# Kernel tuning notes

Hardware: AMD Instinct MI355X
Metric: run time of the kernel (lower is better)

Reference implementation:

```python
import jax, jax.numpy as jnp
import numpy as np

N_NODES = 100000
N_EDGES = 3200000
D = 16
L = 3


def setup_inputs() -> dict:
    key = jax.random.key(0)
    ks = jax.random.split(key, 7)
    scale = 1.0 / np.sqrt(D)
    x = jax.random.normal(ks[0], (N_NODES, D), dtype=jnp.float32)
    edge_index = jax.random.randint(ks[1], (2, N_EDGES), 0, N_NODES, dtype=jnp.int64)
    Wl = jax.random.normal(ks[2], (L, D, D), dtype=jnp.float32) * scale
    bl = jax.random.normal(ks[3], (L, D), dtype=jnp.float32) * scale
    Wr = jax.random.normal(ks[4], (L, D, D), dtype=jnp.float32) * scale
    Wlin = jax.random.normal(ks[5], (L, D, D), dtype=jnp.float32) * scale
    blin = jax.random.normal(ks[6], (L, D), dtype=jnp.float32) * scale
    return {"x": x, "edge_index": edge_index, "Wl": Wl, "bl": bl,
            "Wr": Wr, "Wlin": Wlin, "blin": blin}


def reference(x, edge_index, Wl, bl, Wr, Wlin, blin):
    src = edge_index[0]
    dst = edge_index[1]
    n = x.shape[0]
    # in-degree for mean aggregation (PyG SAGEConv aggr='mean')
    deg = jax.ops.segment_sum(jnp.ones((src.shape[0],), dtype=x.dtype), dst,
                              num_segments=n)
    denom = jnp.maximum(deg, 1.0)[:, None]  # nodes with no in-edges -> 0 agg
    for i in range(Wl.shape[0]):
        # gather source features, scatter-mean onto targets
        agg = jax.ops.segment_sum(x[src], dst, num_segments=n) / denom
        conv = agg @ Wl[i].T + bl[i] + x @ Wr[i].T  # SAGEConv: lin_l(agg)+lin_r(x)
        x = conv + x @ Wlin[i].T + blin[i]          # + Linear residual
    return x
```

## Files before the change

### kernel.cpp

```cpp
#include <hip/hip_runtime.h>

#define N_NODES 100000
#define N_EDGES 3200000
#define D 16
#define L 3

#define TILE 128
#define NB ((N_NODES + TILE - 1) / TILE)
#define CAP 4608
#define NBLK 500
#define SEG (N_EDGES / NBLK)
#define BINT 1024
#define LT 512

__device__ __forceinline__ unsigned packbf(float a, float b) {
    unsigned ua = __float_as_uint(a); ua += 0x7FFFu + ((ua >> 16) & 1u);
    unsigned ub = __float_as_uint(b); ub += 0x7FFFu + ((ub >> 16) & 1u);
    return (ua >> 16) | (ub & 0xFFFF0000u);
}
#define BLO(u) __uint_as_float((u) << 16)
#define BHI(u) __uint_as_float((u) & 0xFFFF0000u)

__global__ void cvt_kernel(const float* __restrict__ x, unsigned* __restrict__ xbf,
                           int* __restrict__ cursor, int n4) {
    int t = blockIdx.x * blockDim.x + threadIdx.x;
    if (t < NB) cursor[t] = 0;
    if (t >= n4) return;
    float4 v = *(const float4*)(x + (size_t)t * 4);
    uint2 o; o.x = packbf(v.x, v.y); o.y = packbf(v.z, v.w);
    *(uint2*)(xbf + (size_t)t * 2) = o;
}

__global__ void bin_scatter(const int* __restrict__ src, const int* __restrict__ dst,
                            int* __restrict__ cursor, unsigned* __restrict__ ebuf, int E) {
    __shared__ int lcnt[NB];
    __shared__ int ldiff[NB];
    __shared__ int lofs[NB];
    __shared__ unsigned sorted[SEG];
    __shared__ unsigned short sbkt[SEG];
    int tid = threadIdx.x;
    for (int i = tid; i < NB; i += BINT) lcnt[i] = 0;
    __syncthreads();
    int b0 = blockIdx.x * SEG, b1 = min(E, b0 + SEG);
    for (int e = b0 + tid * 4; e < b1; e += BINT * 4) {
        int4 d4 = *(const int4*)(dst + e);
        atomicAdd(&lcnt[d4.x >> 7], 1);
        atomicAdd(&lcnt[d4.y >> 7], 1);
        atomicAdd(&lcnt[d4.z >> 7], 1);
        atomicAdd(&lcnt[d4.w >> 7], 1);
    }
    __syncthreads();
    {
        int v = (tid < NB) ? lcnt[tid] : 0;
        sorted[tid] = (unsigned)v;
        __syncthreads();
        for (int off = 1; off < BINT; off <<= 1) {
            unsigned t = (tid >= off) ? sorted[tid - off] : 0u;
            __syncthreads();
            sorted[tid] += t;
            __syncthreads();
        }
        if (tid < NB) {
            int incl = (int)sorted[tid];
            int excl = incl - v;
            lofs[tid] = excl;
            int g = v ? (tid * CAP + atomicAdd(&cursor[tid], v)) : 0;
            ldiff[tid] = g - excl;
            lcnt[tid] = excl;
        }
        __syncthreads();
    }
    for (int e = b0 + tid * 4; e < b1; e += BINT * 4) {
        int4 d4 = *(const int4*)(dst + e);
        int4 s4 = *(const int4*)(src + e);
        int b_, pos;
        b_ = d4.x >> 7; pos = atomicAdd(&lcnt[b_], 1);
        sorted[pos] = ((unsigned)(d4.x & 127) << 17) | (unsigned)s4.x; sbkt[pos] = (unsigned short)b_;
        b_ = d4.y >> 7; pos = atomicAdd(&lcnt[b_], 1);
        sorted[pos] = ((unsigned)(d4.y & 127) << 17) | (unsigned)s4.y; sbkt[pos] = (unsigned short)b_;
        b_ = d4.z >> 7; pos = atomicAdd(&lcnt[b_], 1);
        sorted[pos] = ((unsigned)(d4.z & 127) << 17) | (unsigned)s4.z; sbkt[pos] = (unsigned short)b_;
        b_ = d4.w >> 7; pos = atomicAdd(&lcnt[b_], 1);
        sorted[pos] = ((unsigned)(d4.w & 127) << 17) | (unsigned)s4.w; sbkt[pos] = (unsigned short)b_;
    }
    __syncthreads();
    int nLoc = b1 - b0;
    for (int i = tid; i < nLoc; i += BINT) {
        int b_ = sbkt[i];
        ebuf[ldiff[b_] + i] = sorted[i];
    }
}

__device__ __forceinline__ void agg_xform(
    const float* __restrict__ xin, const unsigned* __restrict__ xbf,
    const unsigned* se2, const int* lofs, int n_loc,
    const float* sWl, const float* sWc, const float* sbc,
    float* __restrict__ xout, unsigned* __restrict__ xbf_out,
    int emit_bf, int b, int N, int tid) {
    int q = tid & 3;
    int n = b * TILE + n_loc;
    if (n >= N) return;

    int s0 = lofs[n_loc];
    int s1 = lofs[n_loc + 1];
    int deg = s1 - s0;

    int lane2 = q >> 1;
    int ho = (q & 1) * 4;

    float acc[8] = {0.f,0.f,0.f,0.f,0.f,0.f,0.f,0.f};
    float bcc[8] = {0.f,0.f,0.f,0.f,0.f,0.f,0.f,0.f};
    int i = s0;
    for (; i + 8 <= s1; i += 8) {
        unsigned p0 = se2[i + 0 + lane2] & 0x1FFFF;
        unsigned p1 = se2[i + 2 + lane2] & 0x1FFFF;
        unsigned p2 = se2[i + 4 + lane2] & 0x1FFFF;
        unsigned p3 = se2[i + 6 + lane2] & 0x1FFFF;
        uint4 g0 = *(const uint4*)(xbf + (size_t)p0 * 8 + ho);
        uint4 g1 = *(const uint4*)(xbf + (size_t)p1 * 8 + ho);
        uint4 g2 = *(const uint4*)(xbf + (size_t)p2 * 8 + ho);
        uint4 g3 = *(const uint4*)(xbf + (size_t)p3 * 8 + ho);
        acc[0] += BLO(g0.x); acc[1] += BHI(g0.x); acc[2] += BLO(g0.y); acc[3] += BHI(g0.y);
        acc[4] += BLO(g0.z); acc[5] += BHI(g0.z); acc[6] += BLO(g0.w); acc[7] += BHI(g0.w);
        bcc[0] += BLO(g1.x); bcc[1] += BHI(g1.x); bcc[2] += BLO(g1.y); bcc[3] += BHI(g1.y);
        bcc[4] += BLO(g1.z); bcc[5] += BHI(g1.z); bcc[6] += BLO(g1.w); bcc[7] += BHI(g1.w);
        acc[0] += BLO(g2.x); acc[1] += BHI(g2.x); acc[2] += BLO(g2.y); acc[3] += BHI(g2.y);
        acc[4] += BLO(g2.z); acc[5] += BHI(g2.z); acc[6] += BLO(g2.w); acc[7] += BHI(g2.w);
        bcc[0] += BLO(g3.x); bcc[1] += BHI(g3.x); bcc[2] += BLO(g3.y); bcc[3] += BHI(g3.y);
        bcc[4] += BLO(g3.z); bcc[5] += BHI(g3.z); bcc[6] += BLO(g3.w); bcc[7] += BHI(g3.w);
    }
    for (; i + 2 <= s1; i += 2) {
        unsigned p = se2[i + lane2] & 0x1FFFF;
        uint4 g = *(const uint4*)(xbf + (size_t)p * 8 + ho);
        acc[0] += BLO(g.x); acc[1] += BHI(g.x); acc[2] += BLO(g.y); acc[3] += BHI(g.y);
        acc[4] += BLO(g.z); acc[5] += BHI(g.z); acc[6] += BLO(g.w); acc[7] += BHI(g.w);
    }
    if (i < s1 && lane2 == 0) {
        unsigned p = se2[i] & 0x1FFFF;
        uint4 g = *(const uint4*)(xbf + (size_t)p * 8 + ho);
        acc[0] += BLO(g.x); acc[1] += BHI(g.x); acc[2] += BLO(g.y); acc[3] += BHI(g.y);
        acc[4] += BLO(g.z); acc[5] += BHI(g.z); acc[6] += BLO(g.w); acc[7] += BHI(g.w);
    }
    #pragma unroll
    for (int k = 0; k < 8; k++) acc[k] += bcc[k];
    #pragma unroll
    for (int k = 0; k < 8; k++) acc[k] += __shfl_xor(acc[k], 2, 4);

    int srcAbs = (tid & 63 & ~3) | (q >> 1);
    float inv = 1.0f / fmaxf((float)deg, 1.0f);
    float a[4];
    #pragma unroll
    for (int k = 0; k < 4; k++) {
        float lo = __shfl(acc[k], srcAbs);
        float hi = __shfl(acc[4 + k], srcAbs);
        a[k] = ((q & 1) ? hi : lo) * inv;
    }

    float4 xq = *(const float4*)(xin + (size_t)n * D + q * 4);
    float xv[4] = { xq.x, xq.y, xq.z, xq.w };

    float o[4];
    #pragma unroll
    for (int j = 0; j < D; j++) {
        float p = 0.f;
        #pragma unroll
        for (int k = 0; k < 4; k++) {
            int kk = q * 4 + k;
            p += a[k] * sWl[j * D + kk] + xv[k] * sWc[j * D + kk];
        }
        p += __shfl_xor(p, 1, 4);
        p += __shfl_xor(p, 2, 4);
        if ((j >> 2) == q) o[j & 3] = p + sbc[j];
    }
    *(float4*)(xout + (size_t)n * D + q * 4) = make_float4(o[0], o[1], o[2], o[3]);
    if (emit_bf) {
        uint2 ob; ob.x = packbf(o[0], o[1]); ob.y = packbf(o[2], o[3]);
        *(uint2*)(xbf_out + (size_t)n * 8 + q * 2) = ob;
    }
}

__global__ void layer0_kernel(const float* __restrict__ xin, const unsigned* __restrict__ xbf,
                              unsigned* __restrict__ ebuf, const int* __restrict__ cnt,
                              int* __restrict__ node_start, int* __restrict__ gperm,
                              const float* __restrict__ Wl, const float* __restrict__ bl,
                              const float* __restrict__ Wr, const float* __restrict__ Wlin,
                              const float* __restrict__ blin,
                              float* __restrict__ xout, unsigned* __restrict__ xbf_out, int N) {
    __shared__ unsigned se[CAP];
    __shared__ unsigned se2[CAP];
    __shared__ int lcnt[TILE];
    __shared__ int sscan[TILE];
    __shared__ int lofs[TILE + 1];
    __shared__ int sdeg[TILE];
    __shared__ int perm[TILE];
    __shared__ float sWl[D * D];
    __shared__ float sWc[D * D];
    __shared__ float sbc[D];

    int tid = threadIdx.x;
    int b = blockIdx.x;
    int base = b * CAP;
    int nE = min(cnt[b], CAP);

    if (tid < D * D) { sWl[tid] = Wl[tid]; sWc[tid] = Wr[tid] + Wlin[tid]; }
    if (tid < D) sbc[tid] = bl[tid] + blin[tid];
    if (tid < TILE) lcnt[tid] = 0;
    __syncthreads();
    for (int i = tid; i < nE; i += LT) {
        unsigned p = ebuf[base + i];
        se[i] = p;
        atomicAdd(&lcnt[p >> 17], 1);
    }
    __syncthreads();
    if (tid < TILE) sscan[tid] = lcnt[tid];
    __syncthreads();
    for (int off = 1; off < TILE; off <<= 1) {
        int t = (tid < TILE && tid >= off) ? sscan[tid - off] : 0;
        __syncthreads();
        if (tid < TILE) sscan[tid] += t;
        __syncthreads();
    }
    if (tid < TILE) {
        int excl = sscan[tid] - lcnt[tid];
        lofs[tid] = excl;
        lcnt[tid] = excl;
        sdeg[tid] = sscan[tid] - excl;
        node_start[b * TILE + tid] = excl;
        if (tid == TILE - 1) lofs[TILE] = sscan[tid];
    }
    __syncthreads();
    if (tid < TILE) {
        int dm = sdeg[tid];
        int r = 0;
        for (int j = 0; j < TILE; j++) {
            int dj = sdeg[j];
            r += (dj > dm) || (dj == dm && j < tid);
        }
        perm[r] = tid;
        gperm[b * TILE + r] = tid;
    }
    for (int i = tid; i < nE; i += LT) {
        unsigned p = se[i];
        int pos = atomicAdd(&lcnt[p >> 17], 1);
        se2[pos] = p;
    }
    __syncthreads();
    for (int i = tid; i < nE; i += LT)
        ebuf[base + i] = se2[i];

    agg_xform(xin, xbf, se2, lofs, perm[tid >> 2], sWl, sWc, sbc,
              xout, xbf_out, 1, b, N, tid);
}

__global__ void layerN_kernel(const float* __restrict__ xin, const unsigned* __restrict__ xbf,
                              const unsigned* __restrict__ ebuf, const int* __restrict__ cnt,
                              const int* __restrict__ node_start, const int* __restrict__ gperm,
                              const float* __restrict__ Wl, const float* __restrict__ bl,
                              const float* __restrict__ Wr, const float* __restrict__ Wlin,
                              const float* __restrict__ blin,
                              float* __restrict__ xout, unsigned* __restrict__ xbf_out,
                              int emit_bf, int N) {
    __shared__ unsigned se2[CAP];
    __shared__ int lofs[TILE + 1];
    __shared__ float sWl[D * D];
    __shared__ float sWc[D * D];
    __shared__ float sbc[D];

    int tid = threadIdx.x;
    int b = blockIdx.x;
    int base = b * CAP;
    int nE = min(cnt[b], CAP);

    if (tid < D * D) { sWl[tid] = Wl[tid]; sWc[tid] = Wr[tid] + Wlin[tid]; }
    if (tid < D) sbc[tid] = bl[tid] + blin[tid];
    if (tid < TILE) lofs[tid] = node_start[b * TILE + tid];
    if (tid == 0) lofs[TILE] = nE;
    for (int i = tid; i < nE; i += LT) se2[i] = ebuf[base + i];
    int n_loc = gperm[b * TILE + (tid >> 2)];
    __syncthreads();

    agg_xform(xin, xbf, se2, lofs, n_loc, sWl, sWc, sbc,
              xout, xbf_out, emit_bf, b, N, tid);
}

extern "C" void kernel_launch(void* const* d_in, const int* in_sizes, int n_in,
                              void* d_out, int out_size, void* d_ws, size_t ws_size,
                              hipStream_t stream) {
    const float* x    = (const float*)d_in[0];
    const int*   ei   = (const int*)d_in[1];
    const float* Wl   = (const float*)d_in[2];
    const float* bl   = (const float*)d_in[3];
    const float* Wr   = (const float*)d_in[4];
    const float* Wlin = (const float*)d_in[5];
    const float* blin = (const float*)d_in[6];
    float* out = (float*)d_out;

    const int* src = ei;
    const int* dst = ei + N_EDGES;

    char* w = (char*)d_ws;
    unsigned* ebuf   = (unsigned*)w;  w += (size_t)NB * CAP * 4;
    float* bufA      = (float*)w;     w += (size_t)N_NODES * D * 4;
    float* bufB      = (float*)w;     w += (size_t)N_NODES * D * 4;
    unsigned* xbf0   = (unsigned*)w;  w += (size_t)N_NODES * 8 * 4;
    unsigned* xbf1   = (unsigned*)w;  w += (size_t)N_NODES * 8 * 4;
    int*   cursor    = (int*)w;       w += (size_t)NB * 4;
    int*   node_start= (int*)w;       w += (size_t)NB * TILE * 4;
    int*   gperm     = (int*)w;       w += (size_t)NB * TILE * 4;

    cvt_kernel<<<(N_NODES * D / 4 + 255) / 256, 256, 0, stream>>>(
        x, xbf0, cursor, N_NODES * D / 4);
    bin_scatter<<<NBLK, BINT, 0, stream>>>(src, dst, cursor, ebuf, N_EDGES);

    layer0_kernel<<<NB, LT, 0, stream>>>(
        x, xbf0, ebuf, cursor, node_start, gperm,
        Wl, bl, Wr, Wlin, blin, bufA, xbf1, N_NODES);
    layerN_kernel<<<NB, LT, 0, stream>>>(
        bufA, xbf1, ebuf, cursor, node_start, gperm,
        Wl + D * D, bl + D, Wr + D * D, Wlin + D * D, blin + D, bufB, xbf0, 1, N_NODES);
    layerN_kernel<<<NB, LT, 0, stream>>>(
        bufB, xbf0, ebuf, cursor, node_start, gperm,
        Wl + 2 * D * D, bl + 2 * D, Wr + 2 * D * D, Wlin + 2 * D * D, blin + 2 * D,
        out, xbf1, 0, N_NODES);
}
```

Measured before the change: 199.5 us.

## Shrink node tiles, fuse bf16 conversion into binning, drop fp32 intermediates

Changes the node tile from 128 to 100 with a smaller per-bucket edge capacity, so buckets use division instead of shifts and 100 of the 128 thread groups do work. Merges the bf16 conversion kernel into the binning kernel as extra blocks and zeroes the cursors with a memset. Intermediate layers now store only bf16 activations and layers 1-2 read their self features from bf16, which removes the fp32 intermediate buffer traffic but adds rounding error. Idle thread groups leave the kernel early.

```diff
diff --git a/kernel.cpp b/kernel.cpp
--- a/kernel.cpp
+++ b/kernel.cpp
@@ -5,12 +5,13 @@
 #define D 16
 #define L 3
 
-#define TILE 128
+#define TILE 100
 #define NB ((N_NODES + TILE - 1) / TILE)
-#define CAP 4608
+#define CAP 3584
 #define NBLK 500
 #define SEG (N_EDGES / NBLK)
 #define BINT 1024
+#define CVTB 391
 #define LT 512
 
 __device__ __forceinline__ unsigned packbf(float a, float b) {
@@ -21,33 +22,35 @@
 #define BLO(u) __uint_as_float((u) << 16)
 #define BHI(u) __uint_as_float((u) & 0xFFFF0000u)
 
-__global__ void cvt_kernel(const float* __restrict__ x, unsigned* __restrict__ xbf,
-                           int* __restrict__ cursor, int n4) {
-    int t = blockIdx.x * blockDim.x + threadIdx.x;
-    if (t < NB) cursor[t] = 0;
-    if (t >= n4) return;
-    float4 v = *(const float4*)(x + (size_t)t * 4);
-    uint2 o; o.x = packbf(v.x, v.y); o.y = packbf(v.z, v.w);
-    *(uint2*)(xbf + (size_t)t * 2) = o;
-}
-
-__global__ void bin_scatter(const int* __restrict__ src, const int* __restrict__ dst,
-                            int* __restrict__ cursor, unsigned* __restrict__ ebuf, int E) {
+__global__ __launch_bounds__(BINT) void pre_kernel(
+        const float* __restrict__ x, unsigned* __restrict__ xbf,
+        const int* __restrict__ src, const int* __restrict__ dst,
+        int* __restrict__ cursor, unsigned* __restrict__ ebuf, int E, int n4) {
     __shared__ int lcnt[NB];
     __shared__ int ldiff[NB];
-    __shared__ int lofs[NB];
     __shared__ unsigned sorted[SEG];
     __shared__ unsigned short sbkt[SEG];
     int tid = threadIdx.x;
+
+    if (blockIdx.x >= NBLK) {
+        int t = (blockIdx.x - NBLK) * BINT + tid;
+        if (t < n4) {
+            float4 v = *(const float4*)(x + (size_t)t * 4);
+            uint2 o; o.x = packbf(v.x, v.y); o.y = packbf(v.z, v.w);
+            *(uint2*)(xbf + (size_t)t * 2) = o;
+        }
+        return;
+    }
+
     for (int i = tid; i < NB; i += BINT) lcnt[i] = 0;
     __syncthreads();
     int b0 = blockIdx.x * SEG, b1 = min(E, b0 + SEG);
     for (int e = b0 + tid * 4; e < b1; e += BINT * 4) {
         int4 d4 = *(const int4*)(dst + e);
-        atomicAdd(&lcnt[d4.x >> 7], 1);
-        atomicAdd(&lcnt[d4.y >> 7], 1);
-        atomicAdd(&lcnt[d4.z >> 7], 1);
-        atomicAdd(&lcnt[d4.w >> 7], 1);
+        atomicAdd(&lcnt[(unsigned)d4.x / TILE], 1);
+        atomicAdd(&lcnt[(unsigned)d4.y / TILE], 1);
+        atomicAdd(&lcnt[(unsigned)d4.z / TILE], 1);
+        atomicAdd(&lcnt[(unsigned)d4.w / TILE], 1);
     }
     __syncthreads();
     {
@@ -61,9 +64,7 @@
             __syncthreads();
         }
         if (tid < NB) {
-            int incl = (int)sorted[tid];
-            int excl = incl - v;
-            lofs[tid] = excl;
+            int excl = (int)sorted[tid] - v;
             int g = v ? (tid * CAP + atomicAdd(&cursor[tid], v)) : 0;
             ldiff[tid] = g - excl;
             lcnt[tid] = excl;
@@ -73,15 +74,15 @@
     for (int e = b0 + tid * 4; e < b1; e += BINT * 4) {
         int4 d4 = *(const int4*)(dst + e);
         int4 s4 = *(const int4*)(src + e);
-        int b_, pos;
-        b_ = d4.x >> 7; pos = atomicAdd(&lcnt[b_], 1);
-        sorted[pos] = ((unsigned)(d4.x & 127) << 17) | (unsigned)s4.x; sbkt[pos] = (unsigned short)b_;
-        b_ = d4.y >> 7; pos = atomicAdd(&lcnt[b_], 1);
-        sorted[pos] = ((unsigned)(d4.y & 127) << 17) | (unsigned)s4.y; sbkt[pos] = (unsigned short)b_;
-        b_ = d4.z >> 7; pos = atomicAdd(&lcnt[b_], 1);
-        sorted[pos] = ((unsigned)(d4.z & 127) << 17) | (unsigned)s4.z; sbkt[pos] = (unsigned short)b_;
-        b_ = d4.w >> 7; pos = atomicAdd(&lcnt[b_], 1);
-        sorted[pos] = ((unsigned)(d4.w & 127) << 17) | (unsigned)s4.w; sbkt[pos] = (unsigned short)b_;
+        unsigned b_; int pos;
+        b_ = (unsigned)d4.x / TILE; pos = atomicAdd(&lcnt[b_], 1);
+        sorted[pos] = ((unsigned)(d4.x - b_ * TILE) << 17) | (unsigned)s4.x; sbkt[pos] = (unsigned short)b_;
+        b_ = (unsigned)d4.y / TILE; pos = atomicAdd(&lcnt[b_], 1);
+        sorted[pos] = ((unsigned)(d4.y - b_ * TILE) << 17) | (unsigned)s4.y; sbkt[pos] = (unsigned short)b_;
+        b_ = (unsigned)d4.z / TILE; pos = atomicAdd(&lcnt[b_], 1);
+        sorted[pos] = ((unsigned)(d4.z - b_ * TILE) << 17) | (unsigned)s4.z; sbkt[pos] = (unsigned short)b_;
+        b_ = (unsigned)d4.w / TILE; pos = atomicAdd(&lcnt[b_], 1);
+        sorted[pos] = ((unsigned)(d4.w - b_ * TILE) << 17) | (unsigned)s4.w; sbkt[pos] = (unsigned short)b_;
     }
     __syncthreads();
     int nLoc = b1 - b0;
@@ -92,7 +93,7 @@
 }
 
 __device__ __forceinline__ void agg_xform(
-    const float* __restrict__ xin, const unsigned* __restrict__ xbf,
+    const float* __restrict__ self_f32, const unsigned* __restrict__ xbf,
     const unsigned* se2, const int* lofs, int n_loc,
     const float* sWl, const float* sWc, const float* sbc,
     float* __restrict__ xout, unsigned* __restrict__ xbf_out,
@@ -156,8 +157,14 @@
         a[k] = ((q & 1) ? hi : lo) * inv;
     }
 
-    float4 xq = *(const float4*)(xin + (size_t)n * D + q * 4);
-    float xv[4] = { xq.x, xq.y, xq.z, xq.w };
+    float xv[4];
+    if (self_f32) {
+        float4 xq = *(const float4*)(self_f32 + (size_t)n * D + q * 4);
+        xv[0] = xq.x; xv[1] = xq.y; xv[2] = xq.z; xv[3] = xq.w;
+    } else {
+        uint2 gx = *(const uint2*)(xbf + (size_t)n * 8 + q * 2);
+        xv[0] = BLO(gx.x); xv[1] = BHI(gx.x); xv[2] = BLO(gx.y); xv[3] = BHI(gx.y);
+    }
 
     float o[4];
     #pragma unroll
@@ -172,20 +179,22 @@
         p += __shfl_xor(p, 2, 4);
         if ((j >> 2) == q) o[j & 3] = p + sbc[j];
     }
-    *(float4*)(xout + (size_t)n * D + q * 4) = make_float4(o[0], o[1], o[2], o[3]);
     if (emit_bf) {
         uint2 ob; ob.x = packbf(o[0], o[1]); ob.y = packbf(o[2], o[3]);
         *(uint2*)(xbf_out + (size_t)n * 8 + q * 2) = ob;
-    }
-}
-
-__global__ void layer0_kernel(const float* __restrict__ xin, const unsigned* __restrict__ xbf,
-                              unsigned* __restrict__ ebuf, const int* __restrict__ cnt,
-                              int* __restrict__ node_start, int* __restrict__ gperm,
-                              const float* __restrict__ Wl, const float* __restrict__ bl,
-                              const float* __restrict__ Wr, const float* __restrict__ Wlin,
-                              const float* __restrict__ blin,
-                              float* __restrict__ xout, unsigned* __restrict__ xbf_out, int N) {
+    } else {
+        *(float4*)(xout + (size_t)n * D + q * 4) = make_float4(o[0], o[1], o[2], o[3]);
+    }
+}
+
+__global__ __launch_bounds__(LT) void layer0_kernel(
+        const float* __restrict__ xin, const unsigned* __restrict__ xbf,
+        unsigned* __restrict__ ebuf, const int* __restrict__ cnt,
+        int* __restrict__ node_start, int* __restrict__ gperm,
+        const float* __restrict__ Wl, const float* __restrict__ bl,
+        const float* __restrict__ Wr, const float* __restrict__ Wlin,
+        const float* __restrict__ blin,
+        unsigned* __restrict__ xbf_out, int N) {
     __shared__ unsigned se[CAP];
     __shared__ unsigned se2[CAP];
     __shared__ int lcnt[TILE];
@@ -248,18 +257,22 @@
     for (int i = tid; i < nE; i += LT)
         ebuf[base + i] = se2[i];
 
-    agg_xform(xin, xbf, se2, lofs, perm[tid >> 2], sWl, sWc, sbc,
-              xout, xbf_out, 1, b, N, tid);
-}
-
-__global__ void layerN_kernel(const float* __restrict__ xin, const unsigned* __restrict__ xbf,
-                              const unsigned* __restrict__ ebuf, const int* __restrict__ cnt,
-                              const int* __restrict__ node_start, const int* __restrict__ gperm,
-                              const float* __restrict__ Wl, const float* __restrict__ bl,
-                              const float* __restrict__ Wr, const float* __restrict__ Wlin,
-                              const float* __restrict__ blin,
-                              float* __restrict__ xout, unsigned* __restrict__ xbf_out,
-                              int emit_bf, int N) {
+    int grp = tid >> 2;
+    int n_loc = (grp < TILE) ? perm[grp] : 0;
+    if (grp >= TILE) return;
+    agg_xform(xin, xbf, se2, lofs, n_loc, sWl, sWc, sbc,
+              nullptr, xbf_out, 1, b, N, tid);
+}
+
+__global__ __launch_bounds__(LT) void layerN_kernel(
+        const unsigned* __restrict__ xbf,
+        const unsigned* __restrict__ ebuf, const int* __restrict__ cnt,
+        const int* __restrict__ node_start, const int* __restrict__ gperm,
+        const float* __restrict__ Wl, const float* __restrict__ bl,
+        const float* __restrict__ Wr, const float* __restrict__ Wlin,
+        const float* __restrict__ blin,
+        float* __restrict__ xout, unsigned* __restrict__ xbf_out,
+        int emit_bf, int N) {
     __shared__ unsigned se2[CAP];
     __shared__ int lofs[TILE + 1];
     __shared__ float sWl[D * D];
@@ -276,10 +289,12 @@
     if (tid < TILE) lofs[tid] = node_start[b * TILE + tid];
     if (tid == 0) lofs[TILE] = nE;
     for (int i = tid; i < nE; i += LT) se2[i] = ebuf[base + i];
-    int n_loc = gperm[b * TILE + (tid >> 2)];
-    __syncthreads();
-
-    agg_xform(xin, xbf, se2, lofs, n_loc, sWl, sWc, sbc,
+    int grp = tid >> 2;
+    int n_loc = (grp < TILE) ? gperm[b * TILE + grp] : 0;
+    __syncthreads();
+
+    if (grp >= TILE) return;
+    agg_xform(nullptr, xbf, se2, lofs, n_loc, sWl, sWc, sbc,
               xout, xbf_out, emit_bf, b, N, tid);
 }
 
@@ -300,26 +315,25 @@
 
     char* w = (char*)d_ws;
     unsigned* ebuf   = (unsigned*)w;  w += (size_t)NB * CAP * 4;
-    float* bufA      = (float*)w;     w += (size_t)N_NODES * D * 4;
-    float* bufB      = (float*)w;     w += (size_t)N_NODES * D * 4;
     unsigned* xbf0   = (unsigned*)w;  w += (size_t)N_NODES * 8 * 4;
     unsigned* xbf1   = (unsigned*)w;  w += (size_t)N_NODES * 8 * 4;
     int*   cursor    = (int*)w;       w += (size_t)NB * 4;
     int*   node_start= (int*)w;       w += (size_t)NB * TILE * 4;
     int*   gperm     = (int*)w;       w += (size_t)NB * TILE * 4;
 
-    cvt_kernel<<<(N_NODES * D / 4 + 255) / 256, 256, 0, stream>>>(
-        x, xbf0, cursor, N_NODES * D / 4);
-    bin_scatter<<<NBLK, BINT, 0, stream>>>(src, dst, cursor, ebuf, N_EDGES);
+    hipMemsetAsync(cursor, 0, (size_t)NB * 4, stream);
+    pre_kernel<<<NBLK + CVTB, BINT, 0, stream>>>(
+        x, xbf0, src, dst, cursor, ebuf, N_EDGES, N_NODES * D / 4);
 
     layer0_kernel<<<NB, LT, 0, stream>>>(
         x, xbf0, ebuf, cursor, node_start, gperm,
-        Wl, bl, Wr, Wlin, blin, bufA, xbf1, N_NODES);
+        Wl, bl, Wr, Wlin, blin, xbf1, N_NODES);
     layerN_kernel<<<NB, LT, 0, stream>>>(
-        bufA, xbf1, ebuf, cursor, node_start, gperm,
-        Wl + D * D, bl + D, Wr + D * D, Wlin + D * D, blin + D, bufB, xbf0, 1, N_NODES);
+        xbf1, ebuf, cursor, node_start, gperm,
+        Wl + D * D, bl + D, Wr + D * D, Wlin + D * D, blin + D,
+        nullptr, xbf0, 1, N_NODES);
     layerN_kernel<<<NB, LT, 0, stream>>>(
-        bufB, xbf0, ebuf, cursor, node_start, gperm,
+        xbf0, ebuf, cursor, node_start, gperm,
         Wl + 2 * D * D, bl + 2 * D, Wr + 2 * D * D, Wlin + 2 * D * D, blin + 2 * D,
-        out, xbf1, 0, N_NODES);
-}
+        out, nullptr, 0, N_NODES);
+}
```

After: 202.6 us. No clear change (+1.6%).

## Merge convert into binning kernel, use wave-shuffle scans, software-pipeline gathers

Applied to the files above, without the earlier changes.

Folds the bf16 conversion into the binning launch as extra blocks, and replaces the cursor reset with a memset. The block-wide Hillis-Steele scans in binning and layer0 become wavefront shuffle scans. The gather loop is software-pipelined, issuing the next group of loads before accumulating the current one, and the x load is hoisted ahead of it. Edge-buffer copies are vectorized to uint4 and launch bounds are added. The intent is to cut launch count, barrier overhead and gather latency, at the cost of higher register pressure from the in-flight loads.

```diff
diff --git a/kernel.cpp b/kernel.cpp
--- a/kernel.cpp
+++ b/kernel.cpp
@@ -3,7 +3,6 @@
 #define N_NODES 100000
 #define N_EDGES 3200000
 #define D 16
-#define L 3
 
 #define TILE 128
 #define NB ((N_NODES + TILE - 1) / TILE)
@@ -11,7 +10,9 @@
 #define NBLK 500
 #define SEG (N_EDGES / NBLK)
 #define BINT 1024
+#define CVTB 391
 #define LT 512
+#define N4 (N_NODES * D / 4)
 
 __device__ __forceinline__ unsigned packbf(float a, float b) {
     unsigned ua = __float_as_uint(a); ua += 0x7FFFu + ((ua >> 16) & 1u);
@@ -21,28 +22,31 @@
 #define BLO(u) __uint_as_float((u) << 16)
 #define BHI(u) __uint_as_float((u) & 0xFFFF0000u)
 
-__global__ void cvt_kernel(const float* __restrict__ x, unsigned* __restrict__ xbf,
-                           int* __restrict__ cursor, int n4) {
-    int t = blockIdx.x * blockDim.x + threadIdx.x;
-    if (t < NB) cursor[t] = 0;
-    if (t >= n4) return;
-    float4 v = *(const float4*)(x + (size_t)t * 4);
-    uint2 o; o.x = packbf(v.x, v.y); o.y = packbf(v.z, v.w);
-    *(uint2*)(xbf + (size_t)t * 2) = o;
-}
-
-__global__ void bin_scatter(const int* __restrict__ src, const int* __restrict__ dst,
-                            int* __restrict__ cursor, unsigned* __restrict__ ebuf, int E) {
+__global__ __launch_bounds__(BINT, 8) void pre_kernel(
+        const float* __restrict__ x, unsigned* __restrict__ xbf,
+        const int* __restrict__ src, const int* __restrict__ dst,
+        int* __restrict__ cursor, unsigned* __restrict__ ebuf) {
     __shared__ int lcnt[NB];
     __shared__ int ldiff[NB];
-    __shared__ int lofs[NB];
     __shared__ unsigned sorted[SEG];
     __shared__ unsigned short sbkt[SEG];
+    __shared__ int wsum[16];
     int tid = threadIdx.x;
+
+    if (blockIdx.x >= NBLK) {
+        int t = (blockIdx.x - NBLK) * BINT + tid;
+        if (t < N4) {
+            float4 v = *(const float4*)(x + (size_t)t * 4);
+            uint2 o; o.x = packbf(v.x, v.y); o.y = packbf(v.z, v.w);
+            *(uint2*)(xbf + (size_t)t * 2) = o;
+        }
+        return;
+    }
+
     for (int i = tid; i < NB; i += BINT) lcnt[i] = 0;
     __syncthreads();
-    int b0 = blockIdx.x * SEG, b1 = min(E, b0 + SEG);
-    for (int e = b0 + tid * 4; e < b1; e += BINT * 4) {
+    int b0 = blockIdx.x * SEG;
+    for (int e = b0 + tid * 4; e < b0 + SEG; e += BINT * 4) {
         int4 d4 = *(const int4*)(dst + e);
         atomicAdd(&lcnt[d4.x >> 7], 1);
         atomicAdd(&lcnt[d4.y >> 7], 1);
@@ -51,26 +55,31 @@
     }
     __syncthreads();
     {
+        int lane = tid & 63, wv = tid >> 6;
         int v = (tid < NB) ? lcnt[tid] : 0;
-        sorted[tid] = (unsigned)v;
+        int s = v;
+        #pragma unroll
+        for (int d_ = 1; d_ < 64; d_ <<= 1) {
+            int u = __shfl_up(s, d_, 64);
+            if (lane >= d_) s += u;
+        }
+        if (lane == 63) wsum[wv] = s;
         __syncthreads();
-        for (int off = 1; off < BINT; off <<= 1) {
-            unsigned t = (tid >= off) ? sorted[tid - off] : 0u;
-            __syncthreads();
-            sorted[tid] += t;
-            __syncthreads();
-        }
+        if (tid == 0) {
+            int a = 0;
+            #pragma unroll
+            for (int i = 0; i < 16; i++) { int t_ = wsum[i]; wsum[i] = a; a += t_; }
+        }
+        __syncthreads();
+        int excl = wsum[wv] + s - v;
         if (tid < NB) {
-            int incl = (int)sorted[tid];
-            int excl = incl - v;
-            lofs[tid] = excl;
             int g = v ? (tid * CAP + atomicAdd(&cursor[tid], v)) : 0;
             ldiff[tid] = g - excl;
             lcnt[tid] = excl;
         }
         __syncthreads();
     }
-    for (int e = b0 + tid * 4; e < b1; e += BINT * 4) {
+    for (int e = b0 + tid * 4; e < b0 + SEG; e += BINT * 4) {
         int4 d4 = *(const int4*)(dst + e);
         int4 s4 = *(const int4*)(src + e);
         int b_, pos;
@@ -84,12 +93,16 @@
         sorted[pos] = ((unsigned)(d4.w & 127) << 17) | (unsigned)s4.w; sbkt[pos] = (unsigned short)b_;
     }
     __syncthreads();
-    int nLoc = b1 - b0;
-    for (int i = tid; i < nLoc; i += BINT) {
+    for (int i = tid; i < SEG; i += BINT) {
         int b_ = sbkt[i];
         ebuf[ldiff[b_] + i] = sorted[i];
     }
 }
+
+#define LDG(j) (*(const uint4*)(xbf + (size_t)(se2[(j) + lane2] & 0x1FFFF) * 8 + ho))
+#define ACC8(g) do { \
+    acc[0] += BLO((g).x); acc[1] += BHI((g).x); acc[2] += BLO((g).y); acc[3] += BHI((g).y); \
+    acc[4] += BLO((g).z); acc[5] += BHI((g).z); acc[6] += BLO((g).w); acc[7] += BHI((g).w); } while (0)
 
 __device__ __forceinline__ void agg_xform(
     const float* __restrict__ xin, const unsigned* __restrict__ xbf,
@@ -101,48 +114,36 @@
     int n = b * TILE + n_loc;
     if (n >= N) return;
 
+    float4 xq = *(const float4*)(xin + (size_t)n * D + q * 4);
+    float xv[4] = { xq.x, xq.y, xq.z, xq.w };
+
     int s0 = lofs[n_loc];
     int s1 = lofs[n_loc + 1];
     int deg = s1 - s0;
-
     int lane2 = q >> 1;
     int ho = (q & 1) * 4;
 
     float acc[8] = {0.f,0.f,0.f,0.f,0.f,0.f,0.f,0.f};
-    float bcc[8] = {0.f,0.f,0.f,0.f,0.f,0.f,0.f,0.f};
+    int end8 = s0 + (deg & ~7);
     int i = s0;
-    for (; i + 8 <= s1; i += 8) {
-        unsigned p0 = se2[i + 0 + lane2] & 0x1FFFF;
-        unsigned p1 = se2[i + 2 + lane2] & 0x1FFFF;
-        unsigned p2 = se2[i + 4 + lane2] & 0x1FFFF;
-        unsigned p3 = se2[i + 6 + lane2] & 0x1FFFF;
-        uint4 g0 = *(const uint4*)(xbf + (size_t)p0 * 8 + ho);
-        uint4 g1 = *(const uint4*)(xbf + (size_t)p1 * 8 + ho);
-        uint4 g2 = *(const uint4*)(xbf + (size_t)p2 * 8 + ho);
-        uint4 g3 = *(const uint4*)(xbf + (size_t)p3 * 8 + ho);
-        acc[0] += BLO(g0.x); acc[1] += BHI(g0.x); acc[2] += BLO(g0.y); acc[3] += BHI(g0.y);
-        acc[4] += BLO(g0.z); acc[5] += BHI(g0.z); acc[6] += BLO(g0.w); acc[7] += BHI(g0.w);
-        bcc[0] += BLO(g1.x); bcc[1] += BHI(g1.x); bcc[2] += BLO(g1.y); bcc[3] += BHI(g1.y);
-        bcc[4] += BLO(g1.z); bcc[5] += BHI(g1.z); bcc[6] += BLO(g1.w); bcc[7] += BHI(g1.w);
-        acc[0] += BLO(g2.x); acc[1] += BHI(g2.x); acc[2] += BLO(g2.y); acc[3] += BHI(g2.y);
-        acc[4] += BLO(g2.z); acc[5] += BHI(g2.z); acc[6] += BLO(g2.w); acc[7] += BHI(g2.w);
-        bcc[0] += BLO(g3.x); bcc[1] += BHI(g3.x); bcc[2] += BLO(g3.y); bcc[3] += BHI(g3.y);
-        bcc[4] += BLO(g3.z); bcc[5] += BHI(g3.z); bcc[6] += BLO(g3.w); bcc[7] += BHI(g3.w);
+    if (i < end8) {
+        uint4 c0 = LDG(i + 0), c1 = LDG(i + 2), c2 = LDG(i + 4), c3 = LDG(i + 6);
+        i += 8;
+        for (; i < end8; i += 8) {
+            uint4 n0 = LDG(i + 0), n1 = LDG(i + 2), n2 = LDG(i + 4), n3 = LDG(i + 6);
+            ACC8(c0); ACC8(c1); ACC8(c2); ACC8(c3);
+            c0 = n0; c1 = n1; c2 = n2; c3 = n3;
+        }
+        ACC8(c0); ACC8(c1); ACC8(c2); ACC8(c3);
     }
     for (; i + 2 <= s1; i += 2) {
-        unsigned p = se2[i + lane2] & 0x1FFFF;
-        uint4 g = *(const uint4*)(xbf + (size_t)p * 8 + ho);
-        acc[0] += BLO(g.x); acc[1] += BHI(g.x); acc[2] += BLO(g.y); acc[3] += BHI(g.y);
-        acc[4] += BLO(g.z); acc[5] += BHI(g.z); acc[6] += BLO(g.w); acc[7] += BHI(g.w);
+        uint4 g = LDG(i);
+        ACC8(g);
     }
     if (i < s1 && lane2 == 0) {
-        unsigned p = se2[i] & 0x1FFFF;
-        uint4 g = *(const uint4*)(xbf + (size_t)p * 8 + ho);
-        acc[0] += BLO(g.x); acc[1] += BHI(g.x); acc[2] += BLO(g.y); acc[3] += BHI(g.y);
-        acc[4] += BLO(g.z); acc[5] += BHI(g.z); acc[6] += BLO(g.w); acc[7] += BHI(g.w);
-    }
-    #pragma unroll
-    for (int k = 0; k < 8; k++) acc[k] += bcc[k];
+        uint4 g = *(const uint4*)(xbf + (size_t)(se2[i] & 0x1FFFF) * 8 + ho);
+        ACC8(g);
+    }
     #pragma unroll
     for (int k = 0; k < 8; k++) acc[k] += __shfl_xor(acc[k], 2, 4);
 
@@ -156,9 +157,6 @@
         a[k] = ((q & 1) ? hi : lo) * inv;
     }
 
-    float4 xq = *(const float4*)(xin + (size_t)n * D + q * 4);
-    float xv[4] = { xq.x, xq.y, xq.z, xq.w };
-
     float o[4];
     #pragma unroll
     for (int j = 0; j < D; j++) {
@@ -179,17 +177,17 @@
     }
 }
 
-__global__ void layer0_kernel(const float* __restrict__ xin, const unsigned* __restrict__ xbf,
-                              unsigned* __restrict__ ebuf, const int* __restrict__ cnt,
-                              int* __restrict__ node_start, int* __restrict__ gperm,
-                              const float* __restrict__ Wl, const float* __restrict__ bl,
-                              const float* __restrict__ Wr, const float* __restrict__ Wlin,
-                              const float* __restrict__ blin,
-                              float* __restrict__ xout, unsigned* __restrict__ xbf_out, int N) {
+__global__ void layer0_kernel(
+        const float* __restrict__ xin, const unsigned* __restrict__ xbf,
+        unsigned* __restrict__ ebuf, const int* __restrict__ cnt,
+        int* __restrict__ node_start, int* __restrict__ gperm,
+        const float* __restrict__ Wl, const float* __restrict__ bl,
+        const float* __restrict__ Wr, const float* __restrict__ Wlin,
+        const float* __restrict__ blin,
+        float* __restrict__ xout, unsigned* __restrict__ xbf_out, int N) {
     __shared__ unsigned se[CAP];
     __shared__ unsigned se2[CAP];
     __shared__ int lcnt[TILE];
-    __shared__ int sscan[TILE];
     __shared__ int lofs[TILE + 1];
     __shared__ int sdeg[TILE];
     __shared__ int perm[TILE];
@@ -201,32 +199,33 @@
     int b = blockIdx.x;
     int base = b * CAP;
     int nE = min(cnt[b], CAP);
+    int nE4 = (nE + 3) >> 2;
 
     if (tid < D * D) { sWl[tid] = Wl[tid]; sWc[tid] = Wr[tid] + Wlin[tid]; }
     if (tid < D) sbc[tid] = bl[tid] + blin[tid];
     if (tid < TILE) lcnt[tid] = 0;
-    __syncthreads();
-    for (int i = tid; i < nE; i += LT) {
-        unsigned p = ebuf[base + i];
-        se[i] = p;
-        atomicAdd(&lcnt[p >> 17], 1);
-    }
-    __syncthreads();
-    if (tid < TILE) sscan[tid] = lcnt[tid];
-    __syncthreads();
-    for (int off = 1; off < TILE; off <<= 1) {
-        int t = (tid < TILE && tid >= off) ? sscan[tid - off] : 0;
-        __syncthreads();
-        if (tid < TILE) sscan[tid] += t;
-        __syncthreads();
-    }
-    if (tid < TILE) {
-        int excl = sscan[tid] - lcnt[tid];
-        lofs[tid] = excl;
-        lcnt[tid] = excl;
-        sdeg[tid] = sscan[tid] - excl;
-        node_start[b * TILE + tid] = excl;
-        if (tid == TILE - 1) lofs[TILE] = sscan[tid];
+    for (int i = tid; i < nE4; i += LT)
+        ((uint4*)se)[i] = ((const uint4*)(ebuf + base))[i];
+    __syncthreads();
+    for (int i = tid; i < nE; i += LT)
+        atomicAdd(&lcnt[se[i] >> 17], 1);
+    __syncthreads();
+    if (tid < 64) {
+        int l2 = tid * 2;
+        int c0 = lcnt[l2], c1 = lcnt[l2 + 1];
+        int v = c0 + c1, s = v;
+        #pragma unroll
+        for (int d_ = 1; d_ < 64; d_ <<= 1) {
+            int u = __shfl_up(s, d_, 64);
+            if (tid >= d_) s += u;
+        }
+        int excl = s - v;
+        lofs[l2] = excl; sdeg[l2] = c0; lcnt[l2] = excl;
+        node_start[b * TILE + l2] = excl;
+        int e1 = excl + c0;
+        lofs[l2 + 1] = e1; sdeg[l2 + 1] = c1; lcnt[l2 + 1] = e1;
+        node_start[b * TILE + l2 + 1] = e1;
+        if (tid == 63) lofs[TILE] = s;
     }
     __syncthreads();
     if (tid < TILE) {
@@ -245,21 +244,22 @@
         se2[pos] = p;
     }
     __syncthreads();
-    for (int i = tid; i < nE; i += LT)
-        ebuf[base + i] = se2[i];
+    for (int i = tid; i < nE4; i += LT)
+        ((uint4*)(ebuf + base))[i] = ((const uint4*)se2)[i];
 
     agg_xform(xin, xbf, se2, lofs, perm[tid >> 2], sWl, sWc, sbc,
               xout, xbf_out, 1, b, N, tid);
 }
 
-__global__ void layerN_kernel(const float* __restrict__ xin, const unsigned* __restrict__ xbf,
-                              const unsigned* __restrict__ ebuf, const int* __restrict__ cnt,
-                              const int* __restrict__ node_start, const int* __restrict__ gperm,
-                              const float* __restrict__ Wl, const float* __restrict__ bl,
-                              const float* __restrict__ Wr, const float* __restrict__ Wlin,
-                              const float* __restrict__ blin,
-                              float* __restrict__ xout, unsigned* __restrict__ xbf_out,
-                              int emit_bf, int N) {
+__global__ __launch_bounds__(LT, 8) void layerN_kernel(
+        const float* __restrict__ xin, const unsigned* __restrict__ xbf,
+        const unsigned* __restrict__ ebuf, const int* __restrict__ cnt,
+        const int* __restrict__ node_start, const int* __restrict__ gperm,
+        const float* __restrict__ Wl, const float* __restrict__ bl,
+        const float* __restrict__ Wr, const float* __restrict__ Wlin,
+        const float* __restrict__ blin,
+        float* __restrict__ xout, unsigned* __restrict__ xbf_out,
+        int emit_bf, int N) {
     __shared__ unsigned se2[CAP];
     __shared__ int lofs[TILE + 1];
     __shared__ float sWl[D * D];
@@ -270,12 +270,14 @@
     int b = blockIdx.x;
     int base = b * CAP;
     int nE = min(cnt[b], CAP);
+    int nE4 = (nE + 3) >> 2;
 
     if (tid < D * D) { sWl[tid] = Wl[tid]; sWc[tid] = Wr[tid] + Wlin[tid]; }
     if (tid < D) sbc[tid] = bl[tid] + blin[tid];
     if (tid < TILE) lofs[tid] = node_start[b * TILE + tid];
     if (tid == 0) lofs[TILE] = nE;
-    for (int i = tid; i < nE; i += LT) se2[i] = ebuf[base + i];
+    for (int i = tid; i < nE4; i += LT)
+        ((uint4*)se2)[i] = ((const uint4*)(ebuf + base))[i];
     int n_loc = gperm[b * TILE + (tid >> 2)];
     __syncthreads();
 
@@ -308,9 +310,8 @@
     int*   node_start= (int*)w;       w += (size_t)NB * TILE * 4;
     int*   gperm     = (int*)w;       w += (size_t)NB * TILE * 4;
 
-    cvt_kernel<<<(N_NODES * D / 4 + 255) / 256, 256, 0, stream>>>(
-        x, xbf0, cursor, N_NODES * D / 4);
-    bin_scatter<<<NBLK, BINT, 0, stream>>>(src, dst, cursor, ebuf, N_EDGES);
+    hipMemsetAsync(cursor, 0, (size_t)NB * 4, stream);
+    pre_kernel<<<NBLK + CVTB, BINT, 0, stream>>>(x, xbf0, src, dst, cursor, ebuf);
 
     layer0_kernel<<<NB, LT, 0, stream>>>(
         x, xbf0, ebuf, cursor, node_start, gperm,
@@ -321,5 +322,5 @@
     layerN_kernel<<<NB, LT, 0, stream>>>(
         bufB, xbf0, ebuf, cursor, node_start, gperm,
         Wl + 2 * D * D, bl + 2 * D, Wr + 2 * D * D, Wlin + 2 * D * D, blin + 2 * D,
-        out, xbf1, 0, N_NODES);
-}
+        out, nullptr, 0, N_NODES);
+}
```

Measured after the change: 192.6 us. 1.04x faster.
